# Optimization experiments

Hardware: AMD Instinct MI355X
Metric: run time of the kernel (lower is better)

## Reference

```python
import jax, jax.numpy as jnp
import numpy as np

SCALING = 2.0  # lora_alpha / r = 32 / 16


def setup_inputs() -> dict:
    key = jax.random.key(0)
    ks = jax.random.split(key, 5)
    N, D, E, R = 8192, 4096, 8, 16
    x = jax.random.normal(ks[0], (N, D), dtype=jnp.float32)
    base_W = jax.random.normal(ks[1], (D, D), dtype=jnp.float32) * (1.0 / np.sqrt(D))
    gate_W = jax.random.normal(ks[2], (E, D), dtype=jnp.float32) * (1.0 / np.sqrt(D))
    A = jax.random.normal(ks[3], (E, R, D), dtype=jnp.float32) * 0.01
    B = jax.random.normal(ks[4], (D, R), dtype=jnp.float32)[None] * jnp.ones((E, 1, 1)) * 0.01
    return {"x": x, "base_W": base_W, "gate_W": gate_W, "A": A, "B": B, "top_k": 2}


def reference(x, base_W, gate_W, A, B, top_k):
    N, D = x.shape
    E = gate_W.shape[0]
    # base linear (torch Linear: y = x @ W.T)
    result = x @ base_W.T
    # gate: top-k logits, softmax over the k selected (in fp32, cast back)
    gate_logits = x @ gate_W.T                      # [N, E]
    top_vals, top_idx = jax.lax.top_k(gate_logits, top_k)  # [N, k]
    w = jax.nn.softmax(top_vals.astype(jnp.float32), axis=-1).astype(x.dtype)
    # dense per-token per-expert routing weight (0 if not selected)
    w_full = jnp.zeros((N, E), dtype=x.dtype).at[
        jnp.arange(N)[:, None], top_idx].add(w)    # [N, E]
    # all-expert LoRA (matches the original dense loop over experts)
    ax = jnp.einsum('nd,erd->ner', x, A)            # [N, E, r]
    bx = jnp.einsum('ner,eor->neo', ax, B)          # [N, E, D]
    result = result + SCALING * jnp.einsum('neo,ne->no', bx, w_full)
    return result
```

## Files before the change

### kernel.cpp

```cpp
#include <hip/hip_runtime.h>
#include <math.h>


#define NTOK 8192
#define DIM  4096
#define NEXP 8
#define RANK 16
#define KAUG (NEXP * RANK)
#define KSPLIT 4
#define NKT  ((DIM + KAUG) / 64)

typedef __bf16 bf16x8 __attribute__((ext_vector_type(8)));
typedef float  f32x4  __attribute__((ext_vector_type(4)));

__device__ __forceinline__ unsigned short f2bf(float f) {
    union { float f; unsigned int u; } v;
    v.f = f;
    unsigned int u = v.u;
    return (unsigned short)((u + 0x7fffu + ((u >> 16) & 1u)) >> 16);
}

__global__ __launch_bounds__(256) void k_cvt(
    const float4* __restrict__ in, ushort4* __restrict__ outv, int n4)
{
    int i = blockIdx.x * 256 + threadIdx.x;
    if (i < n4) {
        float4 v = in[i];
        outv[i] = make_ushort4(f2bf(v.x), f2bf(v.y), f2bf(v.z), f2bf(v.w));
    }
}

__global__ __launch_bounds__(256) void k_bt(
    const float* __restrict__ B, ushort4* __restrict__ Bt4)
{
    int i4 = blockIdx.x * 256 + threadIdx.x;
    int idx = i4 * 4;
    int o = idx >> 7;
    int j = idx & 127;
    int e = j >> 4;
    int r = j & 15;
    const float4 v = *(const float4*)(B + ((size_t)e * DIM + o) * RANK + r);
    Bt4[i4] = make_ushort4(f2bf(v.x), f2bf(v.y), f2bf(v.z), f2bf(v.w));
}

__global__ __launch_bounds__(256) void k_gate(
    const float* __restrict__ x,
    const float* __restrict__ gW,
    float4* __restrict__ gate_out,
    ushort4* __restrict__ xb4)
{
    const int wave = threadIdx.x >> 6;
    const int lane = threadIdx.x & 63;
    const int n0 = blockIdx.x * 16 + wave * 4;

    const float4* __restrict__ g4 = (const float4*)gW;
    const float4* xr0 = (const float4*)(x + (size_t)(n0 + 0) * DIM);
    const float4* xr1 = (const float4*)(x + (size_t)(n0 + 1) * DIM);
    const float4* xr2 = (const float4*)(x + (size_t)(n0 + 2) * DIM);
    const float4* xr3 = (const float4*)(x + (size_t)(n0 + 3) * DIM);
    ushort4* xw0 = xb4 + (size_t)(n0 + 0) * (DIM / 4);
    ushort4* xw1 = xb4 + (size_t)(n0 + 1) * (DIM / 4);
    ushort4* xw2 = xb4 + (size_t)(n0 + 2) * (DIM / 4);
    ushort4* xw3 = xb4 + (size_t)(n0 + 3) * (DIM / 4);

    float s[4][8];
    #pragma unroll
    for (int t = 0; t < 4; ++t)
        #pragma unroll
        for (int e = 0; e < 8; ++e) s[t][e] = 0.f;

    for (int j = 0; j < 16; ++j) {
        const int idx = j * 64 + lane;
        float4 v0 = xr0[idx];
        float4 v1 = xr1[idx];
        float4 v2 = xr2[idx];
        float4 v3 = xr3[idx];
        #pragma unroll
        for (int e = 0; e < 8; ++e) {
            const float4 g = g4[e * (DIM / 4) + idx];
            s[0][e] += v0.x * g.x + v0.y * g.y + v0.z * g.z + v0.w * g.w;
            s[1][e] += v1.x * g.x + v1.y * g.y + v1.z * g.z + v1.w * g.w;
            s[2][e] += v2.x * g.x + v2.y * g.y + v2.z * g.z + v2.w * g.w;
            s[3][e] += v3.x * g.x + v3.y * g.y + v3.z * g.z + v3.w * g.w;
        }
        xw0[idx] = make_ushort4(f2bf(v0.x), f2bf(v0.y), f2bf(v0.z), f2bf(v0.w));
        xw1[idx] = make_ushort4(f2bf(v1.x), f2bf(v1.y), f2bf(v1.z), f2bf(v1.w));
        xw2[idx] = make_ushort4(f2bf(v2.x), f2bf(v2.y), f2bf(v2.z), f2bf(v2.w));
        xw3[idx] = make_ushort4(f2bf(v3.x), f2bf(v3.y), f2bf(v3.z), f2bf(v3.w));
    }

    #pragma unroll
    for (int t = 0; t < 4; ++t)
        #pragma unroll
        for (int e = 0; e < 8; ++e)
            #pragma unroll
            for (int off = 32; off; off >>= 1)
                s[t][e] += __shfl_xor(s[t][e], off);

    #pragma unroll
    for (int t = 0; t < 4; ++t) {
        if (lane == t) {
            int e0 = 0; float v0 = s[t][0];
            #pragma unroll
            for (int e = 1; e < 8; ++e)
                if (s[t][e] > v0) { v0 = s[t][e]; e0 = e; }
            int e1 = -1; float v1 = -INFINITY;
            #pragma unroll
            for (int e = 0; e < 8; ++e)
                if (e != e0 && s[t][e] > v1) { v1 = s[t][e]; e1 = e; }
            float b = __expf(v1 - v0);
            float w0 = 1.f / (1.f + b);
            float w1 = 1.f - w0;
            gate_out[n0 + t] = make_float4((float)e0, (float)e1, w0, w1);
        }
    }
}

__device__ __forceinline__ void stage_lds(
    const unsigned short* gbase, int strideElems,
    unsigned short* ldsBase, int wave, int lane)
{
    const int l8 = lane >> 3;
    const int c8 = ((lane & 7) ^ l8) << 3;
    #pragma unroll
    for (int q = 0; q < 4; ++q) {
        const int r = wave * 32 + q * 8;
        const unsigned short* gp = gbase + (size_t)(r + l8) * strideElems + c8;
        unsigned short* lp = ldsBase + r * 64;
        __builtin_amdgcn_global_load_lds(
            (const __attribute__((address_space(1))) void*)gp,
            (__attribute__((address_space(3))) void*)lp,
            16, 0, 0);
    }
}

__device__ __forceinline__ void mfma_step(
    const unsigned short* As, const unsigned short* Bs,
    int waveM, int waveN, int lane, f32x4 acc[4][4])
{
    const int quad = lane >> 4;
    const int l15  = lane & 15;
    const int x7   = l15 & 7;
    #pragma unroll
    for (int s = 0; s < 2; ++s) {
        const int chunk = (s << 2) | quad;
        const int po = ((chunk ^ x7) << 3);
        bf16x8 af[4], bfv[4];
        #pragma unroll
        for (int i = 0; i < 4; ++i)
            af[i] = *(const bf16x8*)(As + (waveM * 64 + i * 16 + l15) * 64 + po);
        #pragma unroll
        for (int j = 0; j < 4; ++j)
            bfv[j] = *(const bf16x8*)(Bs + (waveN * 64 + j * 16 + l15) * 64 + po);
        #pragma unroll
        for (int i = 0; i < 4; ++i)
            #pragma unroll
            for (int j = 0; j < 4; ++j)
                acc[i][j] = __builtin_amdgcn_mfma_f32_16x16x32_bf16(
                    af[i], bfv[j], acc[i][j], 0, 0, 0);
    }
}

__global__ __launch_bounds__(256) void k_ax(
    const unsigned short* __restrict__ xb,
    const unsigned short* __restrict__ Ab,
    float* __restrict__ axPart)
{
    __shared__ __align__(16) unsigned short As[128 * 64];
    __shared__ __align__(16) unsigned short Bs[128 * 64];
    const int tid  = threadIdx.x;
    const int wave = tid >> 6, lane = tid & 63;
    const int waveM = wave >> 1, waveN = wave & 1;
    const int rowBase = blockIdx.x * 128;
    const int ks = blockIdx.y;
    const int k0 = ks * (DIM / KSPLIT);

    f32x4 acc[4][4] = {};

    for (int it = 0; it < (DIM / KSPLIT) / 64; ++it) {
        stage_lds(xb + (size_t)rowBase * DIM + k0 + it * 64, DIM, As, wave, lane);
        stage_lds(Ab + (size_t)0 * DIM       + k0 + it * 64, DIM, Bs, wave, lane);
        __syncthreads();
        mfma_step(As, Bs, waveM, waveN, lane, acc);
        __syncthreads();
    }

    float* outp = axPart + (size_t)ks * NTOK * KAUG;
    const int quad = lane >> 4, l15 = lane & 15;
    #pragma unroll
    for (int i = 0; i < 4; ++i) {
        #pragma unroll
        for (int j = 0; j < 4; ++j) {
            const int gc = waveN * 64 + j * 16 + l15;
            #pragma unroll
            for (int t = 0; t < 4; ++t) {
                const int gr = rowBase + waveM * 64 + i * 16 + quad * 4 + t;
                outp[(size_t)gr * KAUG + gc] = acc[i][j][t];
            }
        }
    }
}

__global__ __launch_bounds__(256) void k_scale(
    const float* __restrict__ axPart,
    const float4* __restrict__ gate_out,
    ushort4* __restrict__ cB4)
{
    int i4 = blockIdx.x * 256 + threadIdx.x;
    int idx = i4 * 4;
    int n = idx >> 7;
    int j = idx & 127;
    float4 s = make_float4(0.f, 0.f, 0.f, 0.f);
    #pragma unroll
    for (int ks = 0; ks < KSPLIT; ++ks) {
        const float4 v = *(const float4*)(axPart + (size_t)ks * NTOK * KAUG + idx);
        s.x += v.x; s.y += v.y; s.z += v.z; s.w += v.w;
    }
    float4 g = gate_out[n];
    int e  = j >> 4;
    int e0 = (int)g.x;
    int e1 = (int)g.y;
    float scale = (e == e0) ? 2.f * g.z : (e == e1) ? 2.f * g.w : 0.f;
    cB4[i4] = make_ushort4(f2bf(scale * s.x), f2bf(scale * s.y),
                           f2bf(scale * s.z), f2bf(scale * s.w));
}

__global__ __launch_bounds__(512) void k_main(
    const unsigned short* __restrict__ xb,
    const unsigned short* __restrict__ Wb,
    const unsigned short* __restrict__ cB,
    const unsigned short* __restrict__ Bt,
    float* __restrict__ out)
{
    __shared__ __align__(16) unsigned short sA[2][256 * 64];
    __shared__ __align__(16) unsigned short sB[2][256 * 64];

    const int tid  = threadIdx.x;
    const int wave = tid >> 6, lane = tid & 63;
    const int wm = wave >> 2, wn = wave & 3;
    const int quad = lane >> 4, l15 = lane & 15;
    const int x7 = l15 & 7;

    const int bid  = blockIdx.x;
    const int xcd  = bid & 7, slot = bid >> 3;
    const int rowBase = (xcd * 4 + (slot & 3)) * 256;
    const int colBase = (slot >> 2) * 256;

    const unsigned short* aMain = xb + (size_t)rowBase * DIM;
    const unsigned short* bMain = Wb + (size_t)colBase * DIM;
    const unsigned short* aLora = cB + (size_t)rowBase * KAUG;
    const unsigned short* bLora = Bt + (size_t)colBase * KAUG;

    const int l8 = lane >> 3;
    const int c8 = ((lane & 7) ^ l8) << 3;

    auto stageT = [&](int t, int half, bool isA) {
        if (t >= NKT) return;
        unsigned short* ldsR = isA ? &sA[t & 1][0] : &sB[t & 1][0];
        const unsigned short* g;
        int stride;
        if (t < DIM / 64) { g = (isA ? aMain : bMain) + t * 64;              stride = DIM;  }
        else              { g = (isA ? aLora : bLora) + (t - DIM / 64) * 64; stride = KAUG; }
        #pragma unroll
        for (int qq = 0; qq < 2; ++qq) {
            const int r0 = half * 128 + qq * 64 + wave * 8;
            const unsigned short* gp = g + (size_t)(r0 + l8) * stride + c8;
            unsigned short* lp = ldsR + r0 * 64;
            __builtin_amdgcn_global_load_lds(
                (const __attribute__((address_space(1))) void*)gp,
                (__attribute__((address_space(3))) void*)lp,
                16, 0, 0);
        }
    };

    f32x4 acc[8][4] = {};

    stageT(0, 0, true);  stageT(0, 1, true);
    stageT(0, 0, false); stageT(0, 1, false);
    __syncthreads();

    for (int k = 0; k < NKT; ++k) {
        const unsigned short* At = &sA[k & 1][0];
        const unsigned short* Bl = &sB[k & 1][0];

        stageT(k + 1, 0, true);  stageT(k + 1, 1, true);
        stageT(k + 1, 0, false); stageT(k + 1, 1, false);

        bf16x8 bFr[4][2];
        #pragma unroll
        for (int nf = 0; nf < 4; ++nf)
            #pragma unroll
            for (int ksl = 0; ksl < 2; ++ksl) {
                const int r  = wn * 64 + nf * 16 + l15;
                const int ch = ksl * 4 + quad;
                bFr[nf][ksl] = *(const bf16x8*)(Bl + r * 64 + ((ch ^ x7) << 3));
            }
        #pragma unroll
        for (int q = 0; q < 4; ++q) {
            bf16x8 aFr[2][2];
            #pragma unroll
            for (int mi = 0; mi < 2; ++mi)
                #pragma unroll
                for (int ksl = 0; ksl < 2; ++ksl) {
                    const int r  = wm * 128 + (q * 2 + mi) * 16 + l15;
                    const int ch = ksl * 4 + quad;
                    aFr[mi][ksl] = *(const bf16x8*)(At + r * 64 + ((ch ^ x7) << 3));
                }
            #pragma unroll
            for (int mi = 0; mi < 2; ++mi)
                #pragma unroll
                for (int nf = 0; nf < 4; ++nf)
                    #pragma unroll
                    for (int ksl = 0; ksl < 2; ++ksl)
                        acc[q * 2 + mi][nf] = __builtin_amdgcn_mfma_f32_16x16x32_bf16(
                            aFr[mi][ksl], bFr[nf][ksl], acc[q * 2 + mi][nf], 0, 0, 0);
        }

        __syncthreads();
    }

    #pragma unroll
    for (int mf = 0; mf < 8; ++mf) {
        #pragma unroll
        for (int nf = 0; nf < 4; ++nf) {
            const int gc = colBase + wn * 64 + nf * 16 + l15;
            #pragma unroll
            for (int t = 0; t < 4; ++t) {
                const int gr = rowBase + wm * 128 + mf * 16 + quad * 4 + t;
                out[(size_t)gr * DIM + gc] = acc[mf][nf][t];
            }
        }
    }
}

extern "C" void kernel_launch(void* const* d_in, const int* in_sizes, int n_in,
                              void* d_out, int out_size, void* d_ws, size_t ws_size,
                              hipStream_t stream) {
    (void)in_sizes; (void)n_in; (void)out_size; (void)ws_size;

    const float* x  = (const float*)d_in[0];
    const float* bW = (const float*)d_in[1];
    const float* gW = (const float*)d_in[2];
    const float* A  = (const float*)d_in[3];
    const float* B  = (const float*)d_in[4];
    float* out = (float*)d_out;

    char* ws = (char*)d_ws;
    float4*         gate_out = (float4*)ws;
    unsigned short* xb = (unsigned short*)(ws + (1u << 17));
    unsigned short* Wb = xb + (size_t)NTOK * DIM;
    unsigned short* Ab = Wb + (size_t)DIM * DIM;
    unsigned short* Bt = Ab + (size_t)KAUG * DIM;
    unsigned short* cB = Bt + (size_t)DIM * KAUG;
    float*      axPart = (float*)(cB + (size_t)NTOK * KAUG);

    k_gate<<<NTOK / 16, 256, 0, stream>>>(x, gW, gate_out, (ushort4*)xb);
    k_cvt <<<(DIM * DIM / 4 + 255) / 256, 256, 0, stream>>>(
        (const float4*)bW, (ushort4*)Wb, DIM * DIM / 4);
    k_cvt <<<(KAUG * DIM / 4 + 255) / 256, 256, 0, stream>>>(
        (const float4*)A, (ushort4*)Ab, KAUG * DIM / 4);
    k_bt  <<<(DIM * KAUG / 4) / 256, 256, 0, stream>>>(B, (ushort4*)Bt);
    k_ax  <<<dim3(NTOK / 128, KSPLIT), 256, 0, stream>>>(xb, Ab, axPart);
    k_scale<<<(NTOK * KAUG / 4) / 256, 256, 0, stream>>>(
        axPart, gate_out, (ushort4*)cB);
    k_main<<<dim3(512), dim3(512), 0, stream>>>(xb, Wb, cB, Bt, out);
}
```

Before: 593.5 us.

## Software-pipeline LDS fragment loads against MFMAs with explicit waitcnt and priority

Restructures the inner k-tile loop into eight phases, each split by k-slice, and double-buffers the A and B register fragments so the LDS reads for the next phase are issued before the current phase's MFMAs. Manual s_waitcnt lgkmcnt values and sched_barriers hold the compiler's ordering in place, and s_setprio raises wave priority around the MFMA bursts. The aim is to hide LDS read latency behind matrix math. The risk is that the hand-set waitcnt counts must match the issued loads exactly, and the global_load_lds staging also counts on lgkm, which could make the waits stricter than intended.

```diff
diff --git a/kernel.cpp b/kernel.cpp
--- a/kernel.cpp
+++ b/kernel.cpp
@@ -273,6 +273,17 @@
         }
     };
 
+    auto aAddr = [&](const unsigned short* At, int mfrag, int ks) {
+        const int r  = wm * 128 + mfrag * 16 + l15;
+        const int ch = ks * 4 + quad;
+        return (const bf16x8*)(At + r * 64 + ((ch ^ x7) << 3));
+    };
+    auto bAddr = [&](const unsigned short* Bl, int nf, int ks) {
+        const int r  = wn * 64 + nf * 16 + l15;
+        const int ch = ks * 4 + quad;
+        return (const bf16x8*)(Bl + r * 64 + ((ch ^ x7) << 3));
+    };
+
     f32x4 acc[8][4] = {};
 
     stageT(0, 0, true);  stageT(0, 1, true);
@@ -286,34 +297,41 @@
         stageT(k + 1, 0, true);  stageT(k + 1, 1, true);
         stageT(k + 1, 0, false); stageT(k + 1, 1, false);
 
-        bf16x8 bFr[4][2];
-        #pragma unroll
-        for (int nf = 0; nf < 4; ++nf)
-            #pragma unroll
-            for (int ksl = 0; ksl < 2; ++ksl) {
-                const int r  = wn * 64 + nf * 16 + l15;
-                const int ch = ksl * 4 + quad;
-                bFr[nf][ksl] = *(const bf16x8*)(Bl + r * 64 + ((ch ^ x7) << 3));
+        bf16x8 bFr[2][4];
+        bf16x8 aF[2][2];
+        #pragma unroll
+        for (int nf = 0; nf < 4; ++nf) bFr[0][nf] = *bAddr(Bl, nf, 0);
+        aF[0][0] = *aAddr(At, 0, 0);
+        aF[0][1] = *aAddr(At, 1, 0);
+
+        #pragma unroll
+        for (int p = 0; p < 8; ++p) {
+            const int q  = p >> 1;
+            const int ks = p & 1;
+            if (p == 0) {
+                #pragma unroll
+                for (int nf = 0; nf < 4; ++nf) bFr[1][nf] = *bAddr(Bl, nf, 1);
+                aF[1][0] = *aAddr(At, 0, 1);
+                aF[1][1] = *aAddr(At, 1, 1);
+            } else if (p < 7) {
+                const int qn  = (p + 1) >> 1;
+                const int ksn = (p + 1) & 1;
+                aF[(p + 1) & 1][0] = *aAddr(At, qn * 2 + 0, ksn);
+                aF[(p + 1) & 1][1] = *aAddr(At, qn * 2 + 1, ksn);
             }
-        #pragma unroll
-        for (int q = 0; q < 4; ++q) {
-            bf16x8 aFr[2][2];
-            #pragma unroll
-            for (int mi = 0; mi < 2; ++mi)
-                #pragma unroll
-                for (int ksl = 0; ksl < 2; ++ksl) {
-                    const int r  = wm * 128 + (q * 2 + mi) * 16 + l15;
-                    const int ch = ksl * 4 + quad;
-                    aFr[mi][ksl] = *(const bf16x8*)(At + r * 64 + ((ch ^ x7) << 3));
-                }
+            if (p == 0)      asm volatile("s_waitcnt lgkmcnt(6)" ::: "memory");
+            else if (p < 7)  asm volatile("s_waitcnt lgkmcnt(2)" ::: "memory");
+            else             asm volatile("s_waitcnt lgkmcnt(0)" ::: "memory");
+            __builtin_amdgcn_sched_barrier(0);
+            __builtin_amdgcn_s_setprio(1);
             #pragma unroll
             for (int mi = 0; mi < 2; ++mi)
                 #pragma unroll
                 for (int nf = 0; nf < 4; ++nf)
-                    #pragma unroll
-                    for (int ksl = 0; ksl < 2; ++ksl)
-                        acc[q * 2 + mi][nf] = __builtin_amdgcn_mfma_f32_16x16x32_bf16(
-                            aFr[mi][ksl], bFr[nf][ksl], acc[q * 2 + mi][nf], 0, 0, 0);
+                    acc[q * 2 + mi][nf] = __builtin_amdgcn_mfma_f32_16x16x32_bf16(
+                        aF[p & 1][mi], bFr[ks][nf], acc[q * 2 + mi][nf], 0, 0, 0);
+            __builtin_amdgcn_s_setprio(0);
+            __builtin_amdgcn_sched_barrier(0);
         }
 
         __syncthreads();
```

Measured after the change: 589.7 us. Within noise of the previous version (-0.6%).

## Load B operand fragments directly from global into registers, dropping B LDS staging

Applied to the files above, without the earlier changes.

The weight (B) tile is no longer staged through shared memory. Each wave now loads its own B fragments straight from global memory into registers, double-buffered across two alternating register sets, with the K loop unrolled by two. This halves LDS usage and removes the LDS write/read traffic for B, which could raise occupancy. The cost is more register pressure and uncoalesced-ish 16-byte global loads, with each column tile re-fetched by the two M-waves that share it (now from L2 instead of LDS), and the global load latency has to be hidden in registers.

```diff
diff --git a/kernel.cpp b/kernel.cpp
--- a/kernel.cpp
+++ b/kernel.cpp
@@ -233,7 +233,6 @@
     float* __restrict__ out)
 {
     __shared__ __align__(16) unsigned short sA[2][256 * 64];
-    __shared__ __align__(16) unsigned short sB[2][256 * 64];
 
     const int tid  = threadIdx.x;
     const int wave = tid >> 6, lane = tid & 63;
@@ -247,20 +246,27 @@
     const int colBase = (slot >> 2) * 256;
 
     const unsigned short* aMain = xb + (size_t)rowBase * DIM;
-    const unsigned short* bMain = Wb + (size_t)colBase * DIM;
     const unsigned short* aLora = cB + (size_t)rowBase * KAUG;
-    const unsigned short* bLora = Bt + (size_t)colBase * KAUG;
+
+    unsigned int bColMain[4], bColLora[4];
+    #pragma unroll
+    for (int nf = 0; nf < 4; ++nf) {
+        const unsigned int col = colBase + wn * 64 + nf * 16 + l15;
+        bColMain[nf] = col * (unsigned int)DIM;
+        bColLora[nf] = col * (unsigned int)KAUG;
+    }
+    const int kk0 = quad * 8;
 
     const int l8 = lane >> 3;
     const int c8 = ((lane & 7) ^ l8) << 3;
 
-    auto stageT = [&](int t, int half, bool isA) {
+    auto stageA = [&](int t, int half) {
         if (t >= NKT) return;
-        unsigned short* ldsR = isA ? &sA[t & 1][0] : &sB[t & 1][0];
+        unsigned short* ldsR = &sA[t & 1][0];
         const unsigned short* g;
         int stride;
-        if (t < DIM / 64) { g = (isA ? aMain : bMain) + t * 64;              stride = DIM;  }
-        else              { g = (isA ? aLora : bLora) + (t - DIM / 64) * 64; stride = KAUG; }
+        if (t < DIM / 64) { g = aMain + t * 64;              stride = DIM;  }
+        else              { g = aLora + (t - DIM / 64) * 64; stride = KAUG; }
         #pragma unroll
         for (int qq = 0; qq < 2; ++qq) {
             const int r0 = half * 128 + qq * 64 + wave * 8;
@@ -273,28 +279,36 @@
         }
     };
 
+    auto loadB = [&](int t, bf16x8 (&bDst)[2][4]) {
+        if (t >= NKT) return;
+        if (t < DIM / 64) {
+            #pragma unroll
+            for (int ks = 0; ks < 2; ++ks)
+                #pragma unroll
+                for (int nf = 0; nf < 4; ++nf)
+                    bDst[ks][nf] = *(const bf16x8*)(
+                        Wb + bColMain[nf] + t * 64 + ks * 32 + kk0);
+        } else {
+            #pragma unroll
+            for (int ks = 0; ks < 2; ++ks)
+                #pragma unroll
+                for (int nf = 0; nf < 4; ++nf)
+                    bDst[ks][nf] = *(const bf16x8*)(
+                        Bt + bColLora[nf] + (t - DIM / 64) * 64 + ks * 32 + kk0);
+        }
+    };
+
     f32x4 acc[8][4] = {};
-
-    stageT(0, 0, true);  stageT(0, 1, true);
-    stageT(0, 0, false); stageT(0, 1, false);
+    bf16x8 bE[2][4], bO[2][4];
+
+    stageA(0, 0); stageA(0, 1);
+    loadB(0, bE);
     __syncthreads();
 
-    for (int k = 0; k < NKT; ++k) {
+    auto tileBody = [&](int k, bf16x8 (&bCur)[2][4], bf16x8 (&bNxt)[2][4]) {
         const unsigned short* At = &sA[k & 1][0];
-        const unsigned short* Bl = &sB[k & 1][0];
-
-        stageT(k + 1, 0, true);  stageT(k + 1, 1, true);
-        stageT(k + 1, 0, false); stageT(k + 1, 1, false);
-
-        bf16x8 bFr[4][2];
-        #pragma unroll
-        for (int nf = 0; nf < 4; ++nf)
-            #pragma unroll
-            for (int ksl = 0; ksl < 2; ++ksl) {
-                const int r  = wn * 64 + nf * 16 + l15;
-                const int ch = ksl * 4 + quad;
-                bFr[nf][ksl] = *(const bf16x8*)(Bl + r * 64 + ((ch ^ x7) << 3));
-            }
+        stageA(k + 1, 0); stageA(k + 1, 1);
+        loadB(k + 1, bNxt);
         #pragma unroll
         for (int q = 0; q < 4; ++q) {
             bf16x8 aFr[2][2];
@@ -313,10 +327,14 @@
                     #pragma unroll
                     for (int ksl = 0; ksl < 2; ++ksl)
                         acc[q * 2 + mi][nf] = __builtin_amdgcn_mfma_f32_16x16x32_bf16(
-                            aFr[mi][ksl], bFr[nf][ksl], acc[q * 2 + mi][nf], 0, 0, 0);
-        }
-
+                            aFr[mi][ksl], bCur[ksl][nf], acc[q * 2 + mi][nf], 0, 0, 0);
+        }
         __syncthreads();
+    };
+
+    for (int k = 0; k < NKT; k += 2) {
+        tileBody(k,     bE, bO);
+        tileBody(k + 1, bO, bE);
     }
 
     #pragma unroll
```

Measured after the change: 724.9 us. 1.22x slower.
